# Performance work log

Measured on AMD Instinct MI355X. Metric: run time of the kernel, lower is better.

Reference implementation:

```python
import jax, jax.numpy as jnp
import numpy as np

SOS_TOKEN = 0
MAX_SEQ_LENGTH = 64
H = 1024   # hidden_size
V = 32000  # output_size (vocab)
B = 64     # batch


def setup_inputs() -> dict:
    key = jax.random.key(0)
    ks = jax.random.split(key, 10)
    s = 1.0 / np.sqrt(H)
    return {
        "encoder_outputs": jax.random.normal(ks[0], (B, 32, H), dtype=jnp.float32),
        "encoder_hidden": jax.random.normal(ks[1], (1, B, H), dtype=jnp.float32),
        "target_tensor": jax.random.randint(ks[2], (B, MAX_SEQ_LENGTH), 0, V),
        "emb": jax.random.normal(ks[3], (V, H), dtype=jnp.float32) * 0.02,
        "W_ih": jax.random.uniform(ks[4], (3 * H, H), minval=-s, maxval=s, dtype=jnp.float32),
        "W_hh": jax.random.uniform(ks[5], (3 * H, H), minval=-s, maxval=s, dtype=jnp.float32),
        "b_ih": jax.random.uniform(ks[6], (3 * H,), minval=-s, maxval=s, dtype=jnp.float32),
        "b_hh": jax.random.uniform(ks[7], (3 * H,), minval=-s, maxval=s, dtype=jnp.float32),
        "W_out": jax.random.uniform(ks[8], (V, H), minval=-s, maxval=s, dtype=jnp.float32),
        "b_out": jax.random.uniform(ks[9], (V,), minval=-s, maxval=s, dtype=jnp.float32),
    }


def reference(encoder_outputs, encoder_hidden, target_tensor,
              emb, W_ih, W_hh, b_ih, b_hh, W_out, b_out):
    # teacher forcing: input at step 0 is SOS, at step i>0 is target[:, i-1]
    bsz = encoder_outputs.shape[0]
    sos = jnp.full((bsz, 1), SOS_TOKEN, dtype=target_tensor.dtype)
    tokens = jnp.concatenate([sos, target_tensor[:, :MAX_SEQ_LENGTH - 1]], axis=1).T  # [T,B]
    h0 = encoder_hidden[0]  # num_layers=1 -> [B,H]

    def step(h, tok):
        x = jax.nn.relu(emb[tok])                       # [B,H] embed + relu
        gi = x @ W_ih.T + b_ih                          # [B,3H]
        gh = h @ W_hh.T + b_hh                          # [B,3H]
        ir, iz, inn = jnp.split(gi, 3, axis=-1)         # PyTorch gate order r,z,n
        hr, hz, hn = jnp.split(gh, 3, axis=-1)
        r = jax.nn.sigmoid(ir + hr)
        z = jax.nn.sigmoid(iz + hz)
        n = jnp.tanh(inn + r * hn)
        h_new = (1.0 - z) * n + z * h
        logits = h_new @ W_out.T + b_out                # [B,V]
        return h_new, logits

    h_final, logits = jax.lax.scan(step, h0, tokens)    # logits: [T,B,V]
    dec_out = jax.nn.log_softmax(jnp.transpose(logits, (1, 0, 2)), axis=-1)  # [B,T,V]
    return dec_out, h_final[None]  # hidden: [num_layers,B,H]
```

## Files before the change

### kernel.cpp

```cpp
#include <hip/hip_runtime.h>
#include <hip/hip_bf16.h>
#include <stdint.h>

#define H 1024
#define BATCH 64
#define TSTEPS 64
#define VOCAB 32000

typedef __attribute__((ext_vector_type(8))) short bf16x8;
typedef __attribute__((ext_vector_type(4))) float f32x4;

__device__ __forceinline__ uint16_t f2b(float f) {
  union { float f; uint32_t u; } v; v.f = f;
  uint32_t u = v.u;
  return (uint16_t)((u + 0x7FFFu + ((u >> 16) & 1u)) >> 16);
}

__device__ __forceinline__ void g2l16(const uint16_t* g, uint16_t* l) {
  __builtin_amdgcn_global_load_lds((const __attribute__((address_space(1))) void*)(g),
                                   (__attribute__((address_space(3))) void*)(l), 16, 0, 0);
}

__global__ void cast_bf16_kernel(const float* __restrict__ src, uint16_t* __restrict__ dst, int n4) {
  int i = blockIdx.x * blockDim.x + threadIdx.x;
  int stride = gridDim.x * blockDim.x;
  for (; i < n4; i += stride) {
    float4 f = ((const float4*)src)[i];
    union { uint16_t u[4]; uint64_t d; } o;
    o.u[0] = f2b(f.x); o.u[1] = f2b(f.y); o.u[2] = f2b(f.z); o.u[3] = f2b(f.w);
    ((uint64_t*)dst)[i] = o.d;
  }
}

__global__ void embed_kernel(const float* __restrict__ emb, const int* __restrict__ tgt,
                             uint16_t* __restrict__ X) {
  int i = blockIdx.x;
  int t = i >> 6, b = i & 63;
  int tok = (t == 0) ? 0 : tgt[b * TSTEPS + (t - 1)];
  const float4* src = (const float4*)(emb + (size_t)tok * H);
  uint64_t* dst = (uint64_t*)(X + (size_t)i * H);
  int k = threadIdx.x;
  float4 f = src[k];
  union { uint16_t u[4]; uint64_t d; } o;
  o.u[0] = f2b(fmaxf(f.x, 0.f)); o.u[1] = f2b(fmaxf(f.y, 0.f));
  o.u[2] = f2b(fmaxf(f.z, 0.f)); o.u[3] = f2b(fmaxf(f.w, 0.f));
  dst[k] = o.d;
}

__global__ void h0_kernel(const float* __restrict__ eh, uint16_t* __restrict__ hb0) {
  int i = blockIdx.x * blockDim.x + threadIdx.x;
  float4 f = ((const float4*)eh)[i];
  union { uint16_t u[4]; uint64_t d; } o;
  o.u[0] = f2b(f.x); o.u[1] = f2b(f.y); o.u[2] = f2b(f.z); o.u[3] = f2b(f.w);
  ((uint64_t*)hb0)[i] = o.d;
}

__global__ __launch_bounds__(256) void gi_gemm_kernel(
    const uint16_t* __restrict__ A,
    const uint16_t* __restrict__ Bm,
    const float* __restrict__ bias,
    float* __restrict__ out) {
  __shared__ uint16_t lA[128 * 32];
  __shared__ uint16_t lB[128 * 32];
  const int tid = threadIdx.x;
  const int lane = tid & 63;
  const int w = tid >> 6;
  const int wr = w >> 1, wc = w & 1;
  int flat = blockIdx.y * 24 + blockIdx.x;
  int nf = (flat & 7) * 96 + (flat >> 3);
  const int m0 = (nf / 24) * 128;
  const int n0 = (nf % 24) * 128;

  f32x4 acc[4][4];
#pragma unroll
  for (int mi = 0; mi < 4; ++mi)
#pragma unroll
    for (int ni = 0; ni < 4; ++ni) acc[mi][ni] = (f32x4){0, 0, 0, 0};

  const int srow = w * 16 + (lane >> 2);
  const int scol = (lane & 3) * 8;

  for (int k0 = 0; k0 < 1024; k0 += 32) {
    __syncthreads();
    g2l16(A + (size_t)(m0 + srow) * 1024 + k0 + scol,       &lA[w * 512]);
    g2l16(A + (size_t)(m0 + 64 + srow) * 1024 + k0 + scol,  &lA[2048 + w * 512]);
    g2l16(Bm + (size_t)(n0 + srow) * 1024 + k0 + scol,      &lB[w * 512]);
    g2l16(Bm + (size_t)(n0 + 64 + srow) * 1024 + k0 + scol, &lB[2048 + w * 512]);
    __syncthreads();
    bf16x8 a[4], b[4];
#pragma unroll
    for (int mi = 0; mi < 4; ++mi)
      a[mi] = *(const bf16x8*)&lA[(wr * 64 + mi * 16 + (lane & 15)) * 32 + (lane >> 4) * 8];
#pragma unroll
    for (int ni = 0; ni < 4; ++ni)
      b[ni] = *(const bf16x8*)&lB[(wc * 64 + ni * 16 + (lane & 15)) * 32 + (lane >> 4) * 8];
#pragma unroll
    for (int mi = 0; mi < 4; ++mi)
#pragma unroll
      for (int ni = 0; ni < 4; ++ni)
        acc[mi][ni] = __builtin_amdgcn_mfma_f32_16x16x32_bf16(a[mi], b[ni], acc[mi][ni], 0, 0, 0);
  }

#pragma unroll
  for (int ni = 0; ni < 4; ++ni) {
    int v = n0 + wc * 64 + ni * 16 + (lane & 15);
    float bv = bias[v];
#pragma unroll
    for (int mi = 0; mi < 4; ++mi) {
#pragma unroll
      for (int r = 0; r < 4; ++r) {
        int row = m0 + wr * 64 + mi * 16 + (lane >> 4) * 4 + r;
        out[(size_t)row * 3072 + v] = acc[mi][ni][r] + bv;
      }
    }
  }
}

__global__ __launch_bounds__(64) void step_kernel(
    const uint16_t* __restrict__ Whh_b,
    const float* __restrict__ gi,
    const float* __restrict__ b_hh,
    const float* __restrict__ h_cur,
    float* __restrict__ h_nxt,
    uint16_t* __restrict__ Hsb,
    int t) {
  const int lane = threadIdx.x;
  const int l15 = lane & 15, kq = lane >> 4;
  const int rg = blockIdx.x >> 6, cs = blockIdx.x & 63;
  const int m0 = rg * 16, c0 = cs * 16;
  const int c = c0 + l15;

  float gr[4], gz[4], gn[4], hold[4];
#pragma unroll
  for (int r = 0; r < 4; ++r) {
    int m = m0 + kq * 4 + r;
    const float* gp = gi + (size_t)(t * 64 + m) * 3072;
    gr[r] = gp[c]; gz[r] = gp[1024 + c]; gn[r] = gp[2048 + c];
    hold[r] = h_cur[(size_t)m * 1024 + c];
  }

  const uint16_t* ap = Hsb + (size_t)(t * 64 + m0 + l15) * 1024 + kq * 8;
  const uint16_t* br = Whh_b + (size_t)(c) * 1024 + kq * 8;
  const uint16_t* bz = Whh_b + (size_t)(1024 + c) * 1024 + kq * 8;
  const uint16_t* bn = Whh_b + (size_t)(2048 + c) * 1024 + kq * 8;

  f32x4 ar = {0,0,0,0}, az = {0,0,0,0}, an = {0,0,0,0};
#pragma unroll
  for (int kk = 0; kk < 32; ++kk) {
    bf16x8 a = *(const bf16x8*)(ap + kk * 32);
    ar = __builtin_amdgcn_mfma_f32_16x16x32_bf16(a, *(const bf16x8*)(br + kk * 32), ar, 0, 0, 0);
    az = __builtin_amdgcn_mfma_f32_16x16x32_bf16(a, *(const bf16x8*)(bz + kk * 32), az, 0, 0, 0);
    an = __builtin_amdgcn_mfma_f32_16x16x32_bf16(a, *(const bf16x8*)(bn + kk * 32), an, 0, 0, 0);
  }

  float bhr = b_hh[c], bhz = b_hh[1024 + c], bhn = b_hh[2048 + c];
#pragma unroll
  for (int r = 0; r < 4; ++r) {
    int m = m0 + kq * 4 + r;
    float rg_ = 1.f / (1.f + __expf(-(gr[r] + ar[r] + bhr)));
    float zg  = 1.f / (1.f + __expf(-(gz[r] + az[r] + bhz)));
    float ng  = tanhf(gn[r] + rg_ * (an[r] + bhn));
    float hnew = (1.f - zg) * ng + zg * hold[r];
    h_nxt[(size_t)m * 1024 + c] = hnew;
    Hsb[(size_t)((t + 1) * 64 + m) * 1024 + c] = f2b(hnew);
  }
}

__global__ __launch_bounds__(256) void out_gemm_kernel(
    const uint16_t* __restrict__ A,
    const uint16_t* __restrict__ Bm,
    const float* __restrict__ bias,
    float* __restrict__ out) {
  __shared__ uint16_t lA[128 * 32];
  __shared__ uint16_t lB[128 * 32];
  const int tid = threadIdx.x;
  const int lane = tid & 63;
  const int w = tid >> 6;
  const int wr = w >> 1, wc = w & 1;
  int flat = blockIdx.y * 250 + blockIdx.x;
  int nf = (flat & 7) * 1000 + (flat >> 3);
  const int m0 = (nf / 250) * 128;
  const int n0 = (nf % 250) * 128;

  f32x4 acc[4][4];
#pragma unroll
  for (int mi = 0; mi < 4; ++mi)
#pragma unroll
    for (int ni = 0; ni < 4; ++ni) acc[mi][ni] = (f32x4){0, 0, 0, 0};

  const int srow = w * 16 + (lane >> 2);
  const int scol = (lane & 3) * 8;

  for (int k0 = 0; k0 < 1024; k0 += 32) {
    __syncthreads();
    g2l16(A + (size_t)(m0 + srow) * 1024 + k0 + scol,       &lA[w * 512]);
    g2l16(A + (size_t)(m0 + 64 + srow) * 1024 + k0 + scol,  &lA[2048 + w * 512]);
    g2l16(Bm + (size_t)(n0 + srow) * 1024 + k0 + scol,      &lB[w * 512]);
    g2l16(Bm + (size_t)(n0 + 64 + srow) * 1024 + k0 + scol, &lB[2048 + w * 512]);
    __syncthreads();
    bf16x8 a[4], b[4];
#pragma unroll
    for (int mi = 0; mi < 4; ++mi)
      a[mi] = *(const bf16x8*)&lA[(wr * 64 + mi * 16 + (lane & 15)) * 32 + (lane >> 4) * 8];
#pragma unroll
    for (int ni = 0; ni < 4; ++ni)
      b[ni] = *(const bf16x8*)&lB[(wc * 64 + ni * 16 + (lane & 15)) * 32 + (lane >> 4) * 8];
#pragma unroll
    for (int mi = 0; mi < 4; ++mi)
#pragma unroll
      for (int ni = 0; ni < 4; ++ni)
        acc[mi][ni] = __builtin_amdgcn_mfma_f32_16x16x32_bf16(a[mi], b[ni], acc[mi][ni], 0, 0, 0);
  }

#pragma unroll
  for (int ni = 0; ni < 4; ++ni) {
    int v = n0 + wc * 64 + ni * 16 + (lane & 15);
    float bv = bias[v];
#pragma unroll
    for (int mi = 0; mi < 4; ++mi) {
#pragma unroll
      for (int r = 0; r < 4; ++r) {
        int row = m0 + wr * 64 + mi * 16 + (lane >> 4) * 4 + r;
        size_t off = (size_t)(row & 63) * (TSTEPS * (size_t)VOCAB)
                   + (size_t)(row >> 6) * VOCAB + v;
        __builtin_nontemporal_store(acc[mi][ni][r] + bv, &out[off]);
      }
    }
  }
}

__global__ __launch_bounds__(256) void lsm_kernel(float* __restrict__ out) {
  float* row = out + (size_t)blockIdx.x * VOCAB;
  const int tid = threadIdx.x;
  float m = -3.4e38f, s = 0.f;
  for (int i = tid * 4; i < VOCAB; i += 1024) {
    float4 x = *(const float4*)(row + i);
    float lm = fmaxf(fmaxf(x.x, x.y), fmaxf(x.z, x.w));
    if (lm > m) { s *= expf(m - lm); m = lm; }
    s += expf(x.x - m) + expf(x.y - m) + expf(x.z - m) + expf(x.w - m);
  }
#pragma unroll
  for (int off = 32; off > 0; off >>= 1) {
    float m2 = __shfl_xor(m, off);
    float s2 = __shfl_xor(s, off);
    float mn = fmaxf(m, m2);
    s = s * expf(m - mn) + s2 * expf(m2 - mn);
    m = mn;
  }
  __shared__ float sm[4], ss[4];
  if ((tid & 63) == 0) { sm[tid >> 6] = m; ss[tid >> 6] = s; }
  __syncthreads();
  float M = fmaxf(fmaxf(sm[0], sm[1]), fmaxf(sm[2], sm[3]));
  float S = ss[0] * expf(sm[0] - M) + ss[1] * expf(sm[1] - M)
          + ss[2] * expf(sm[2] - M) + ss[3] * expf(sm[3] - M);
  float lse = M + logf(S);
  for (int i = tid * 4; i < VOCAB; i += 1024) {
    f32x4 x = *(const f32x4*)(row + i);
    x[0] -= lse; x[1] -= lse; x[2] -= lse; x[3] -= lse;
    __builtin_nontemporal_store(x, (f32x4*)(row + i));
  }
}

__global__ void hcopy_kernel(const float* __restrict__ h, float* __restrict__ out) {
  int i = blockIdx.x * blockDim.x + threadIdx.x;
  ((float4*)out)[i] = ((const float4*)h)[i];
}

extern "C" void kernel_launch(void* const* d_in, const int* in_sizes, int n_in,
                              void* d_out, int out_size, void* d_ws, size_t ws_size,
                              hipStream_t stream) {
  const float* enc_hidden = (const float*)d_in[1];
  const int* tgt          = (const int*)d_in[2];
  const float* emb        = (const float*)d_in[3];
  const float* W_ih       = (const float*)d_in[4];
  const float* W_hh       = (const float*)d_in[5];
  const float* b_ih       = (const float*)d_in[6];
  const float* b_hh       = (const float*)d_in[7];
  const float* W_out      = (const float*)d_in[8];
  const float* b_out      = (const float*)d_in[9];
  float* out = (float*)d_out;

  char* ws = (char*)d_ws;
  float*    gi     = (float*)(ws);
  uint16_t* Wout_b = (uint16_t*)(ws);
  uint16_t* Wih_b  = (uint16_t*)(ws + 65536000);
  uint16_t* Whh_b  = (uint16_t*)(ws + 71827456);
  uint16_t* Xb     = (uint16_t*)(ws + 78118912);
  uint16_t* Hsb    = (uint16_t*)(ws + 86507520);
  float*    hA     = (float*)   (ws + 95027200);
  float*    hB     = (float*)   (ws + 95289344);

  cast_bf16_kernel<<<2048, 256, 0, stream>>>(W_ih, Wih_b, 3072 * 1024 / 4);
  cast_bf16_kernel<<<2048, 256, 0, stream>>>(W_hh, Whh_b, 3072 * 1024 / 4);
  embed_kernel<<<4096, 256, 0, stream>>>(emb, tgt, Xb);
  h0_kernel<<<64, 256, 0, stream>>>(enc_hidden, Hsb);

  dim3 gg(24, 32);
  gi_gemm_kernel<<<gg, 256, 0, stream>>>(Xb, Wih_b, b_ih, gi);

  for (int t = 0; t < TSTEPS; ++t) {
    const float* hc = (t == 0) ? enc_hidden : ((t & 1) ? hA : hB);
    float* hn       = (t & 1) ? hB : hA;
    step_kernel<<<256, 64, 0, stream>>>(Whh_b, gi, b_hh, hc, hn, Hsb, t);
  }

  cast_bf16_kernel<<<2048, 256, 0, stream>>>(W_out, Wout_b, VOCAB * 1024 / 4);

  dim3 g(250, 32);
  out_gemm_kernel<<<g, 256, 0, stream>>>(Hsb + 65536, Wout_b, b_out, out);
  lsm_kernel<<<4096, 256, 0, stream>>>(out);
  hcopy_kernel<<<64, 256, 0, stream>>>((TSTEPS & 1) ? hB : hA, out + 131072000ull);
}
```

Measured before the change: 1.166 ms.

## Fuse partial log-softmax statistics into output GEMM epilogue, finalize with light pass

The output GEMM epilogue now computes per-row max and sum-of-exp over each 128-column tile and writes these partials to a workspace buffer that reuses the embedding scratch region. A new finalize kernel reduces the 250 partials per row into the log-sum-exp and then subtracts it in one read-modify-write pass. The old two-read pass over the 524 MB logits is dropped. The block-to-tile mapping is also reordered so each XCD covers a band of rows. The cost is extra epilogue work, shuffles and shared memory in the GEMM.

```diff
diff --git a/kernel.cpp b/kernel.cpp
--- a/kernel.cpp
+++ b/kernel.cpp
@@ -170,17 +170,20 @@
     const uint16_t* __restrict__ A,
     const uint16_t* __restrict__ Bm,
     const float* __restrict__ bias,
-    float* __restrict__ out) {
+    float* __restrict__ out,
+    float2* __restrict__ px) {
   __shared__ uint16_t lA[128 * 32];
   __shared__ uint16_t lB[128 * 32];
+  __shared__ float smax[128][2];
+  __shared__ float ssum[128][2];
   const int tid = threadIdx.x;
   const int lane = tid & 63;
   const int w = tid >> 6;
   const int wr = w >> 1, wc = w & 1;
   int flat = blockIdx.y * 250 + blockIdx.x;
-  int nf = (flat & 7) * 1000 + (flat >> 3);
-  const int m0 = (nf / 250) * 128;
-  const int n0 = (nf % 250) * 128;
+  int xcd = flat & 7, i = flat >> 3;
+  const int m0 = ((xcd << 2) | (i & 3)) * 128;
+  const int n0 = (i >> 2) * 128;
 
   f32x4 acc[4][4];
 #pragma unroll
@@ -212,48 +215,94 @@
         acc[mi][ni] = __builtin_amdgcn_mfma_f32_16x16x32_bf16(a[mi], b[ni], acc[mi][ni], 0, 0, 0);
   }
 
+  float bv[4], rmax[4][4], rsum[4][4];
+#pragma unroll
+  for (int mi = 0; mi < 4; ++mi)
+#pragma unroll
+    for (int r = 0; r < 4; ++r) { rmax[mi][r] = -3.4e38f; rsum[mi][r] = 0.f; }
+
 #pragma unroll
   for (int ni = 0; ni < 4; ++ni) {
     int v = n0 + wc * 64 + ni * 16 + (lane & 15);
-    float bv = bias[v];
+    bv[ni] = bias[v];
 #pragma unroll
     for (int mi = 0; mi < 4; ++mi) {
 #pragma unroll
       for (int r = 0; r < 4; ++r) {
+        float x = acc[mi][ni][r] + bv[ni];
         int row = m0 + wr * 64 + mi * 16 + (lane >> 4) * 4 + r;
         size_t off = (size_t)(row & 63) * (TSTEPS * (size_t)VOCAB)
                    + (size_t)(row >> 6) * VOCAB + v;
-        __builtin_nontemporal_store(acc[mi][ni][r] + bv, &out[off]);
+        __builtin_nontemporal_store(x, &out[off]);
+        rmax[mi][r] = fmaxf(rmax[mi][r], x);
       }
     }
   }
-}
-
-__global__ __launch_bounds__(256) void lsm_kernel(float* __restrict__ out) {
-  float* row = out + (size_t)blockIdx.x * VOCAB;
+#pragma unroll
+  for (int mask = 1; mask < 16; mask <<= 1)
+#pragma unroll
+    for (int mi = 0; mi < 4; ++mi)
+#pragma unroll
+      for (int r = 0; r < 4; ++r)
+        rmax[mi][r] = fmaxf(rmax[mi][r], __shfl_xor(rmax[mi][r], mask));
+#pragma unroll
+  for (int ni = 0; ni < 4; ++ni)
+#pragma unroll
+    for (int mi = 0; mi < 4; ++mi)
+#pragma unroll
+      for (int r = 0; r < 4; ++r)
+        rsum[mi][r] += __expf(acc[mi][ni][r] + bv[ni] - rmax[mi][r]);
+#pragma unroll
+  for (int mask = 1; mask < 16; mask <<= 1)
+#pragma unroll
+    for (int mi = 0; mi < 4; ++mi)
+#pragma unroll
+      for (int r = 0; r < 4; ++r)
+        rsum[mi][r] += __shfl_xor(rsum[mi][r], mask);
+
+  if ((lane & 15) == 0) {
+    int kq = lane >> 4;
+#pragma unroll
+    for (int mi = 0; mi < 4; ++mi)
+#pragma unroll
+      for (int r = 0; r < 4; ++r) {
+        int rl = wr * 64 + mi * 16 + kq * 4 + r;
+        smax[rl][wc] = rmax[mi][r];
+        ssum[rl][wc] = rsum[mi][r];
+      }
+  }
+  __syncthreads();
+  if (tid < 128) {
+    float m0v = smax[tid][0], m1v = smax[tid][1];
+    float M = fmaxf(m0v, m1v);
+    float S = ssum[tid][0] * __expf(m0v - M) + ssum[tid][1] * __expf(m1v - M);
+    px[(size_t)(m0 + tid) * 256 + (n0 >> 7)] = make_float2(M, S);
+  }
+}
+
+__global__ __launch_bounds__(256) void lsefin_kernel(
+    const float2* __restrict__ px, float* __restrict__ out) {
   const int tid = threadIdx.x;
+  const int b = blockIdx.x >> 6, t = blockIdx.x & 63;
+  const float2* p = px + (size_t)(t * 64 + b) * 256;
   float m = -3.4e38f, s = 0.f;
-  for (int i = tid * 4; i < VOCAB; i += 1024) {
-    float4 x = *(const float4*)(row + i);
-    float lm = fmaxf(fmaxf(x.x, x.y), fmaxf(x.z, x.w));
-    if (lm > m) { s *= expf(m - lm); m = lm; }
-    s += expf(x.x - m) + expf(x.y - m) + expf(x.z - m) + expf(x.w - m);
-  }
-#pragma unroll
-  for (int off = 32; off > 0; off >>= 1) {
+  if (tid < 250) { float2 v = p[tid]; m = v.x; s = v.y; }
+#pragma unroll
+  for (int off = 1; off < 64; off <<= 1) {
     float m2 = __shfl_xor(m, off);
     float s2 = __shfl_xor(s, off);
     float mn = fmaxf(m, m2);
-    s = s * expf(m - mn) + s2 * expf(m2 - mn);
+    s = s * __expf(m - mn) + s2 * __expf(m2 - mn);
     m = mn;
   }
   __shared__ float sm[4], ss[4];
   if ((tid & 63) == 0) { sm[tid >> 6] = m; ss[tid >> 6] = s; }
   __syncthreads();
   float M = fmaxf(fmaxf(sm[0], sm[1]), fmaxf(sm[2], sm[3]));
-  float S = ss[0] * expf(sm[0] - M) + ss[1] * expf(sm[1] - M)
-          + ss[2] * expf(sm[2] - M) + ss[3] * expf(sm[3] - M);
+  float S = ss[0] * __expf(sm[0] - M) + ss[1] * __expf(sm[1] - M)
+          + ss[2] * __expf(sm[2] - M) + ss[3] * __expf(sm[3] - M);
   float lse = M + logf(S);
+  float* row = out + (size_t)blockIdx.x * VOCAB;
   for (int i = tid * 4; i < VOCAB; i += 1024) {
     f32x4 x = *(const f32x4*)(row + i);
     x[0] -= lse; x[1] -= lse; x[2] -= lse; x[3] -= lse;
@@ -286,6 +335,7 @@
   uint16_t* Wih_b  = (uint16_t*)(ws + 65536000);
   uint16_t* Whh_b  = (uint16_t*)(ws + 71827456);
   uint16_t* Xb     = (uint16_t*)(ws + 78118912);
+  float2*   px     = (float2*)  (ws + 78118912);
   uint16_t* Hsb    = (uint16_t*)(ws + 86507520);
   float*    hA     = (float*)   (ws + 95027200);
   float*    hB     = (float*)   (ws + 95289344);
@@ -307,7 +357,7 @@
   cast_bf16_kernel<<<2048, 256, 0, stream>>>(W_out, Wout_b, VOCAB * 1024 / 4);
 
   dim3 g(250, 32);
-  out_gemm_kernel<<<g, 256, 0, stream>>>(Hsb + 65536, Wout_b, b_out, out);
-  lsm_kernel<<<4096, 256, 0, stream>>>(out);
+  out_gemm_kernel<<<g, 256, 0, stream>>>(Hsb + 65536, Wout_b, b_out, out, px);
+  lsefin_kernel<<<4096, 256, 0, stream>>>(px, out);
   hcopy_kernel<<<64, 256, 0, stream>>>((TSTEPS & 1) ? hB : hA, out + 131072000ull);
 }
```

After: 1.115 ms. -4.4%, faster.
